# Optimization experiments

Measured on AMD Instinct MI355X. Metric: run time of the kernel, lower is better.

## Reference

```python
import jax, jax.numpy as jnp
import numpy as np

L, D, H, B, SX, SY, VS, VT = 6, 1024, 16, 4, 512, 512, 32000, 32000
DK = D // H
FF = 4 * D
EPS = 1e-3          # LayerNorm eps (added to std, not var)
SCALE_EMB = float(np.sqrt(D))
NEG = -1e30         # stands in for -inf; fully-masked rows are zeroed after softmax


def pos_encoding(length, d):
    # tensor2tensor-style sinusoid: [sin | cos] concatenated along channels
    nt = d // 2
    lti = np.log(1e4) / (nt - 1)
    inv = np.exp(np.arange(nt) * -lti)
    st = np.arange(length)[:, None] * inv[None, :]
    return jnp.asarray(np.concatenate([np.sin(st), np.cos(st)], axis=1), jnp.float32)


def layer_norm(z, a, b):
    # faithful to the torch module: uses unbiased std (ddof=1) and divides by (std + eps)
    mu = z.mean(-1, keepdims=True)
    sig = jnp.sqrt(((z - mu) ** 2).sum(-1, keepdims=True) / (z.shape[-1] - 1))
    return (z - mu) / (sig + EPS) * a + b


def mha(xq, xkv, wq, wk, wv, wo, mask):
    # xq: (b, lq, D), xkv: (b, lk, D); head-chunking of channel dim == reshape to (H, DK)
    b, lq, _ = xq.shape
    q = (xq @ wq.T).reshape(b, lq, H, DK)
    k = (xkv @ wk.T).reshape(b, -1, H, DK)
    v = (xkv @ wv.T).reshape(b, -1, H, DK)
    s = jnp.einsum('bqhd,bkhd->bhqk', q, k) * (1.0 / np.sqrt(DK))
    m = mask[:, None, :, :]
    s = jnp.where(m, s, NEG)
    att = jax.nn.softmax(s, axis=-1)
    att = att * m.any(-1, keepdims=True)  # replicates NaN->0 for fully masked rows
    c = jnp.einsum('bhqk,bkhd->bqhd', att, v).reshape(b, lq, D)
    return c @ wo.T


def setup_inputs():
    key = jax.random.key(0)
    ks = jax.random.split(key, 10)
    s = 0.02
    emb_x = (jax.random.normal(ks[0], (VS, D), jnp.float32) * s).at[0].set(0.0)  # padding_idx=0
    emb_y = (jax.random.normal(ks[1], (VT, D), jnp.float32) * s).at[0].set(0.0)
    return {
        'emb_x': emb_x, 'emb_y': emb_y,
        'enc_qkvo': jax.random.normal(ks[2], (L, 4, D, D), jnp.float32) * s,
        'enc_ln_s': jnp.ones((L, 2, D), jnp.float32), 'enc_ln_b': jnp.zeros((L, 2, D), jnp.float32),
        'enc_w1': jax.random.normal(ks[3], (L, FF, D), jnp.float32) * s, 'enc_b1': jnp.zeros((L, FF), jnp.float32),
        'enc_w2': jax.random.normal(ks[4], (L, D, FF), jnp.float32) * s, 'enc_b2': jnp.zeros((L, D), jnp.float32),
        'dec_qkvo': jax.random.normal(ks[5], (L, 8, D, D), jnp.float32) * s,
        'dec_ln_s': jnp.ones((L, 3, D), jnp.float32), 'dec_ln_b': jnp.zeros((L, 3, D), jnp.float32),
        'dec_w1': jax.random.normal(ks[6], (L, FF, D), jnp.float32) * s, 'dec_b1': jnp.zeros((L, FF), jnp.float32),
        'dec_w2': jax.random.normal(ks[7], (L, D, FF), jnp.float32) * s, 'dec_b2': jnp.zeros((L, D), jnp.float32),
        'x_block': jax.random.randint(ks[8], (B, SX), 0, VS),
        'y_block': jax.random.randint(ks[9], (B, SY), 0, VT),
    }


def reference(emb_x, emb_y, enc_qkvo, enc_ln_s, enc_ln_b, enc_w1, enc_b1, enc_w2, enc_b2,
              dec_qkvo, dec_ln_s, dec_ln_b, dec_w1, dec_b1, dec_w2, dec_b2, x_block, y_block):
    # internal layout (b, len, D); torch code uses (b, D, len) -- math is identical
    ex = emb_x[x_block] * SCALE_EMB + pos_encoding(SX, D)[None]
    ey = emb_y[y_block] * SCALE_EMB + pos_encoding(SY, D)[None]
    xv = x_block != 0
    yv = y_block != 0
    xx = xv[:, :, None] & xv[:, None, :]                                   # (B, qx, kx)
    xy = yv[:, :, None] & xv[:, None, :]                                   # (B, qy, kx)
    yy = (yv[:, :, None] & yv[:, None, :]) & jnp.tril(jnp.ones((SY, SY), bool))[None]
    e = ex
    for i in range(L):
        sub = mha(e, e, enc_qkvo[i, 0], enc_qkvo[i, 1], enc_qkvo[i, 2], enc_qkvo[i, 3], xx)
        e = layer_norm(e + sub, enc_ln_s[i, 0], enc_ln_b[i, 0])
        sub = jax.nn.relu(e @ enc_w1[i].T + enc_b1[i]) @ enc_w2[i].T + enc_b2[i]
        e = layer_norm(e + sub, enc_ln_s[i, 1], enc_ln_b[i, 1])
    z = e
    e = ey
    for i in range(L):
        sub = mha(e, e, dec_qkvo[i, 0], dec_qkvo[i, 1], dec_qkvo[i, 2], dec_qkvo[i, 3], yy)
        e = layer_norm(e + sub, dec_ln_s[i, 0], dec_ln_b[i, 0])
        sub = mha(e, z, dec_qkvo[i, 4], dec_qkvo[i, 5], dec_qkvo[i, 6], dec_qkvo[i, 7], xy)
        e = layer_norm(e + sub, dec_ln_s[i, 1], dec_ln_b[i, 1])
        sub = jax.nn.relu(e @ dec_w1[i].T + dec_b1[i]) @ dec_w2[i].T + dec_b2[i]
        e = layer_norm(e + sub, dec_ln_s[i, 2], dec_ln_b[i, 2])
    return e @ emb_y.T  # tied output projection -> (B, SY, VT)
```

## Files before the change

kernel.cpp:

```cpp
#include <hip/hip_runtime.h>

typedef unsigned short u16;
typedef float f32x4 __attribute__((ext_vector_type(4)));
typedef __bf16 bf16x8 __attribute__((ext_vector_type(8)));
typedef u16 u16x8 __attribute__((ext_vector_type(8)));

#define DEV __device__ __forceinline__

DEV u16 f2bf(float f) {
  unsigned u = __builtin_bit_cast(unsigned, f);
  u += 0x7fffu + ((u >> 16) & 1u);
  return (u16)(u >> 16);
}

DEV float wsum(float v) {
#pragma unroll
  for (int o = 32; o > 0; o >>= 1) v += __shfl_xor(v, o, 64);
  return v;
}
DEV float gmax16(float v) {
#pragma unroll
  for (int o = 8; o > 0; o >>= 1) v = fmaxf(v, __shfl_xor(v, o, 64));
  return v;
}
DEV float gsum16(float v) {
#pragma unroll
  for (int o = 8; o > 0; o >>= 1) v += __shfl_xor(v, o, 64);
  return v;
}

DEV void gld16(const void* g, void* l) {
  __builtin_amdgcn_global_load_lds((const __attribute__((address_space(1))) void*)g,
                                   (__attribute__((address_space(3))) void*)l, 16, 0, 0);
}

template <int N>
DEV void vwait() {
  if constexpr (N == 0) asm volatile("s_waitcnt vmcnt(0)" ::: "memory");
  else if constexpr (N == 2) asm volatile("s_waitcnt vmcnt(2)" ::: "memory");
  else if constexpr (N == 4) asm volatile("s_waitcnt vmcnt(4)" ::: "memory");
  else asm volatile("s_waitcnt vmcnt(6)" ::: "memory");
}

DEV void remap_bxy(int& bx, int& by) {
  const int gx = gridDim.x, gy = gridDim.y;
  const int flat = blockIdx.y * gx + blockIdx.x;
  const int nwg = gx * gy;
  const int q = nwg >> 3, r = nwg & 7;
  const int xcd = flat & 7, li = flat >> 3;
  const int wg = (xcd < r ? xcd * (q + 1) : r * (q + 1) + (xcd - r) * q) + li;
  by = wg % gy;
  bx = wg / gy;
}

template <int BM, int BN, int MODE, int W, int BK>
__global__ __launch_bounds__(256, W) void gemm_k(
    const u16* __restrict__ A, const u16* __restrict__ B, int lda, int ldb, int K,
    float alpha, const float* __restrict__ bias, const float* __restrict__ resid,
    float* __restrict__ Cf, int ldc, u16* __restrict__ Cb, u16* __restrict__ qp,
    u16* __restrict__ kp, u16* __restrict__ vp, int n_off) {
  constexpr int FM = BM / 32, FN = BN / 32;
  constexpr int CHA = BM / 8, CHT = (BM + BN) / 8;
  constexpr int KCH = BK / 64;
  __shared__ u16 lds[2][(BM + BN) * BK];
  const int lane = threadIdx.x & 63, wid = threadIdx.x >> 6;
  const int wr = wid >> 1, wc = wid & 1;
  int bx, by;
  remap_bxy(bx, by);
  const u16* gA = A + (long)(by * BM) * lda;
  const u16* gB = B + (long)(bx * BN) * ldb;

  const f32x4 zero4 = {0.f, 0.f, 0.f, 0.f};
  f32x4 acc[FM][FN];
#pragma unroll
  for (int m = 0; m < FM; ++m)
#pragma unroll
    for (int n = 0; n < FN; ++n) acc[m][n] = zero4;

  const int r8 = lane >> 3, sl = lane & 7;

  auto stage = [&](int buf, int kt) {
#pragma unroll
    for (int sub = 0; sub < KCH; ++sub) {
      const int kb = kt * BK + (sub << 6);
      u16* lbase = &lds[buf][sub * (BM + BN) * 64];
#pragma unroll
      for (int c0 = 0; c0 < CHT; c0 += 4) {
        const int c = c0 + wid;
        u16* l = lbase + (c << 9);
        const u16* g;
        if (c < CHA) {
          int r = (c << 3) + r8;
          g = gA + (long)r * lda + kb + ((sl ^ (r & 7)) << 3);
        } else {
          int r = ((c - CHA) << 3) + r8;
          g = gB + (long)r * ldb + kb + ((sl ^ (r & 7)) << 3);
        }
        gld16(g, l);
      }
    }
  };

  const int KT = K / BK;
  stage(0, 0);
  __syncthreads();
  int cur = 0;
  for (int kt = 0; kt < KT; ++kt) {
    if (kt + 1 < KT) stage(cur ^ 1, kt + 1);
#pragma unroll
    for (int q = 0; q < 2 * KCH; ++q) {
      const int kh = q >> 1, kl = q & 1;
      const u16* lA = &lds[cur][kh * (BM + BN) * 64];
      const u16* lB = lA + (BM << 6);
      bf16x8 af[FM], bv[FN];
#pragma unroll
      for (int m = 0; m < FM; ++m) {
        int r = wr * (BM / 2) + m * 16 + (lane & 15);
        int slot = ((kl << 2) | (lane >> 4)) ^ (r & 7);
        af[m] = *(const bf16x8*)(lA + (r << 6) + (slot << 3));
      }
#pragma unroll
      for (int n = 0; n < FN; ++n) {
        int r = wc * (BN / 2) + n * 16 + (lane & 15);
        int slot = ((kl << 2) | (lane >> 4)) ^ (r & 7);
        bv[n] = *(const bf16x8*)(lB + (r << 6) + (slot << 3));
      }
#pragma unroll
      for (int m = 0; m < FM; ++m)
#pragma unroll
        for (int n = 0; n < FN; ++n)
          acc[m][n] = __builtin_amdgcn_mfma_f32_16x16x32_bf16(af[m], bv[n], acc[m][n], 0, 0, 0);
    }
    __syncthreads();
    cur ^= 1;
  }

  const int rb = by * BM + wr * (BM / 2) + ((lane >> 4) << 2);
  const int cb = bx * BN + wc * (BN / 2) + (lane & 15);
  if constexpr (MODE == 2) {
    const bool isV = (bx * BN + n_off) >= 2048;
    if (isV) {
      __syncthreads();
      u16* T = (u16*)&lds[0][0];
      constexpr int TS = BM + 8;
#pragma unroll
      for (int m = 0; m < FM; ++m)
#pragma unroll
        for (int n = 0; n < FN; ++n) {
          int cl = wc * (BN / 2) + n * 16 + (lane & 15);
#pragma unroll
          for (int j = 0; j < 4; ++j) {
            int rl = wr * (BM / 2) + m * 16 + ((lane >> 4) << 2) + j;
            T[cl * TS + rl] = f2bf(acc[m][n][j]);
          }
        }
      __syncthreads();
      const int vcb = bx * BN + n_off - 2048;
      const int b = (by * BM) >> 9, s0 = (by * BM) & 511;
#pragma unroll
      for (int p = 0; p < BM * BN / 2048; ++p) {
        int idx = p * 2048 + threadIdx.x * 8;
        int dl = idx / BM, slx = idx & (BM - 1);
        u16x8 o;
#pragma unroll
        for (int e = 0; e < 8; ++e) o[e] = T[dl * TS + slx + e];
        int vc = vcb + dl;
        *(u16x8*)(vp + (((long)b * 16 + (vc >> 6)) * 64 + (vc & 63)) * 512 + s0 + slx) = o;
      }
    } else {
#pragma unroll
      for (int m = 0; m < FM; ++m)
#pragma unroll
        for (int n = 0; n < FN; ++n)
#pragma unroll
          for (int j = 0; j < 4; ++j) {
            const int row = rb + m * 16 + j;
            const int np = cb + n * 16 + n_off;
            const int sel = np >> 10, dim = np & 1023;
            long base = (((long)(row >> 9) * 16 + (dim >> 6)) * 512 + (row & 511)) * 64 + (dim & 63);
            u16 val = f2bf(acc[m][n][j]);
            if (sel == 0) qp[base] = val;
            else kp[base] = val;
          }
    }
  } else {
#pragma unroll
    for (int m = 0; m < FM; ++m)
#pragma unroll
      for (int n = 0; n < FN; ++n)
#pragma unroll
        for (int j = 0; j < 4; ++j) {
          const int row = rb + m * 16 + j;
          const int col = cb + n * 16;
          float v = acc[m][n][j];
          if constexpr (MODE == 0) {
            float r = v * alpha;
            if (bias) r += bias[col];
            if (resid) r += resid[(long)row * ldc + col];
            Cf[(long)row * ldc + col] = r;
          } else {
            Cb[(long)row * ldc + col] = f2bf(fmaxf(v + bias[col], 0.f));
          }
        }
  }
}

__global__ __launch_bounds__(512, 1) void gemm256_k(
    const u16* __restrict__ A, const u16* __restrict__ B, int lda, int ldb, int K,
    float* __restrict__ Cf, int ldc) {
  __shared__ u16 As[2][256 * 64];
  __shared__ u16 Bs[2][256 * 64];
  const int lane = threadIdx.x & 63, wid = threadIdx.x >> 6;
  const int wr = wid >> 2, wc = wid & 3;
  int bx, by;
  remap_bxy(bx, by);
  const u16* gA = A + (long)(by * 256) * lda;
  const u16* gB = B + (long)(bx * 256) * ldb;

  const f32x4 z4 = {0.f, 0.f, 0.f, 0.f};
  f32x4 acc[8][4];
#pragma unroll
  for (int m = 0; m < 8; ++m)
#pragma unroll
    for (int n = 0; n < 4; ++n) acc[m][n] = z4;

  const int ssl = lane & 7;

  auto stageH = [&](int t, int h) {
    const int kb = t << 6;
    const int buf = t & 1;
    const bool isA = (h == 0) || (h == 3);
    u16* ldsb = isA ? &As[buf][0] : &Bs[buf][0];
    const u16* gsrc = isA ? gA : gB;
    const int ld = isA ? lda : ldb;
    const int rbase = (h >= 2) ? 128 : 0;
#pragma unroll
    for (int rr = 0; rr < 2; ++rr) {
      const int r0 = rbase + rr * 64 + (wid << 3);
      const int r = r0 + (lane >> 3);
      gld16(gsrc + (long)r * ld + kb + ((ssl ^ (r & 7)) << 3), ldsb + (r0 << 6));
    }
  };

  const int KT = K >> 6;
  stageH(0, 0);
  stageH(0, 1);
  stageH(0, 2);
  stageH(0, 3);

  for (int t = 0; t < KT; ++t) {
    const int buf = t & 1;
    const bool more = (t + 1 < KT);
    const u16* lA = &As[buf][0];
    const u16* lB = &Bs[buf][0];
    bf16x8 af[4][2], bvl[2][2], bvh[2][2];

    vwait<4>();
    __builtin_amdgcn_s_barrier();
    __builtin_amdgcn_sched_barrier(0);
#pragma unroll
    for (int m = 0; m < 4; ++m)
#pragma unroll
      for (int kk = 0; kk < 2; ++kk) {
        int r = wr * 64 + m * 16 + (lane & 15);
        int sg = ((kk << 2) | (lane >> 4)) ^ (r & 7);
        af[m][kk] = *(const bf16x8*)(lA + (r << 6) + (sg << 3));
      }
#pragma unroll
    for (int n = 0; n < 2; ++n)
#pragma unroll
      for (int kk = 0; kk < 2; ++kk) {
        int c = wc * 32 + n * 16 + (lane & 15);
        int sg = ((kk << 2) | (lane >> 4)) ^ (c & 7);
        bvl[n][kk] = *(const bf16x8*)(lB + (c << 6) + (sg << 3));
      }
    if (more) stageH(t + 1, 0);
    __builtin_amdgcn_s_setprio(1);
#pragma unroll
    for (int kk = 0; kk < 2; ++kk)
#pragma unroll
      for (int m = 0; m < 4; ++m)
#pragma unroll
        for (int n = 0; n < 2; ++n)
          acc[m][n] = __builtin_amdgcn_mfma_f32_16x16x32_bf16(af[m][kk], bvl[n][kk], acc[m][n], 0, 0, 0);
    __builtin_amdgcn_s_setprio(0);

    if (more) vwait<4>();
    else vwait<2>();
    __builtin_amdgcn_s_barrier();
    __builtin_amdgcn_sched_barrier(0);
#pragma unroll
    for (int n = 0; n < 2; ++n)
#pragma unroll
      for (int kk = 0; kk < 2; ++kk) {
        int c = 128 + wc * 32 + n * 16 + (lane & 15);
        int sg = ((kk << 2) | (lane >> 4)) ^ (c & 7);
        bvh[n][kk] = *(const bf16x8*)(lB + (c << 6) + (sg << 3));
      }
    if (more) stageH(t + 1, 1);
    __builtin_amdgcn_s_setprio(1);
#pragma unroll
    for (int kk = 0; kk < 2; ++kk)
#pragma unroll
      for (int m = 0; m < 4; ++m)
#pragma unroll
        for (int n = 0; n < 2; ++n)
          acc[m][2 + n] = __builtin_amdgcn_mfma_f32_16x16x32_bf16(af[m][kk], bvh[n][kk], acc[m][2 + n], 0, 0, 0);
    __builtin_amdgcn_s_setprio(0);

    if (more) vwait<4>();
    else vwait<0>();
    __builtin_amdgcn_s_barrier();
    __builtin_amdgcn_sched_barrier(0);
#pragma unroll
    for (int m = 0; m < 4; ++m)
#pragma unroll
      for (int kk = 0; kk < 2; ++kk) {
        int r = 128 + wr * 64 + m * 16 + (lane & 15);
        int sg = ((kk << 2) | (lane >> 4)) ^ (r & 7);
        af[m][kk] = *(const bf16x8*)(lA + (r << 6) + (sg << 3));
      }
    if (more) stageH(t + 1, 2);
    __builtin_amdgcn_s_setprio(1);
#pragma unroll
    for (int kk = 0; kk < 2; ++kk)
#pragma unroll
      for (int m = 0; m < 4; ++m)
#pragma unroll
        for (int n = 0; n < 2; ++n)
          acc[4 + m][2 + n] = __builtin_amdgcn_mfma_f32_16x16x32_bf16(af[m][kk], bvh[n][kk], acc[4 + m][2 + n], 0, 0, 0);
    __builtin_amdgcn_s_setprio(0);

    __builtin_amdgcn_s_barrier();
    __builtin_amdgcn_sched_barrier(0);
    if (more) stageH(t + 1, 3);
    __builtin_amdgcn_s_setprio(1);
#pragma unroll
    for (int kk = 0; kk < 2; ++kk)
#pragma unroll
      for (int m = 0; m < 4; ++m)
#pragma unroll
        for (int n = 0; n < 2; ++n)
          acc[4 + m][n] = __builtin_amdgcn_mfma_f32_16x16x32_bf16(af[m][kk], bvl[n][kk], acc[4 + m][n], 0, 0, 0);
    __builtin_amdgcn_s_setprio(0);
  }

  const int rb = by * 256 + wr * 64 + ((lane >> 4) << 2);
  const int cb = bx * 256 + wc * 32 + (lane & 15);
#pragma unroll
  for (int mi = 0; mi < 8; ++mi)
#pragma unroll
    for (int ni = 0; ni < 4; ++ni)
#pragma unroll
      for (int j = 0; j < 4; ++j) {
        int row = rb + (mi & 3) * 16 + ((mi >> 2) << 7) + j;
        int col = cb + (ni & 1) * 16 + ((ni >> 1) << 7);
        Cf[(long)row * ldc + col] = acc[mi][ni][j];
      }
}

template <int CAUSAL>
__global__ __launch_bounds__(512, 2) void fattn_k(
    const u16* __restrict__ Qg, const u16* __restrict__ Kg, const u16* __restrict__ Vtg,
    const int* __restrict__ qids, const int* __restrict__ kids, u16* __restrict__ ctx) {
  __shared__ u16 Qs[128 * 64];
  __shared__ u16 Ks[2][64 * 64];
  __shared__ u16 Vs[2][64 * 64];
  __shared__ u16 Ps[8][16 * 64];
  const int lane = threadIdx.x & 63, wid = threadIdx.x >> 6;
  const int qt = blockIdx.x, bh = blockIdx.y, b = bh >> 4, h = bh & 15;
  const int q0 = qt << 7;
  const u16* Qbase = Qg + ((long)bh * 512 + q0) * 64;
  const u16* Kbase = Kg + (long)bh * 512 * 64;
  const u16* Vbase = Vtg + (long)bh * 64 * 512;
  const int r8 = lane >> 3, sl = lane & 7;

#pragma unroll
  for (int c0 = 0; c0 < 16; c0 += 8) {
    int c = c0 + wid;
    int r = (c << 3) + r8;
    gld16(Qbase + (long)r * 64 + ((sl ^ (r & 7)) << 3), &Qs[c << 9]);
  }

  auto stageKV = [&](int buf, int kt) {
#pragma unroll
    for (int c0 = 0; c0 < 16; c0 += 8) {
      int c = c0 + wid;
      if (c < 8) {
        int r = (c << 3) + r8;
        gld16(Kbase + (long)(kt * 64 + r) * 64 + ((sl ^ (r & 7)) << 3), &Ks[buf][c << 9]);
      } else {
        int r = ((c - 8) << 3) + r8;
        gld16(Vbase + (long)r * 512 + kt * 64 + ((sl ^ (r & 7)) << 3), &Vs[buf][(c - 8) << 9]);
      }
    }
  };

  const int NKT = CAUSAL ? ((q0 >> 6) + 2) : 8;
  stageKV(0, 0);
  __syncthreads();

  const f32x4 z4 = {0.f, 0.f, 0.f, 0.f};
  f32x4 oacc[4];
  float mrun[4], lrun[4];
  bool qv[4];
#pragma unroll
  for (int j = 0; j < 4; ++j) {
    mrun[j] = -3e38f;
    lrun[j] = 0.f;
    int qg = q0 + wid * 16 + ((lane >> 4) << 2) + j;
    qv[j] = qids[(b << 9) + qg] != 0;
  }
#pragma unroll
  for (int nd = 0; nd < 4; ++nd) oacc[nd] = z4;

  int cur = 0;
  for (int kt = 0; kt < NKT; ++kt) {
    if (kt + 1 < NKT) stageKV(cur ^ 1, kt + 1);
    f32x4 s[4];
#pragma unroll
    for (int n = 0; n < 4; ++n) s[n] = z4;
    __builtin_amdgcn_s_setprio(1);
#pragma unroll
    for (int kk = 0; kk < 2; ++kk) {
      bf16x8 aq, bk[4];
      int r = wid * 16 + (lane & 15);
      int slot = ((kk << 2) | (lane >> 4)) ^ (r & 7);
      aq = *(const bf16x8*)&Qs[(r << 6) + (slot << 3)];
#pragma unroll
      for (int n = 0; n < 4; ++n) {
        int c = n * 16 + (lane & 15);
        int slt = ((kk << 2) | (lane >> 4)) ^ (c & 7);
        bk[n] = *(const bf16x8*)&Ks[cur][(c << 6) + (slt << 3)];
      }
#pragma unroll
      for (int n = 0; n < 4; ++n)
        s[n] = __builtin_amdgcn_mfma_f32_16x16x32_bf16(aq, bk[n], s[n], 0, 0, 0);
    }
    __builtin_amdgcn_s_setprio(0);
    bool kvld[4];
#pragma unroll
    for (int n = 0; n < 4; ++n)
      kvld[n] = kids[(b << 9) + (kt << 6) + (n << 4) + (lane & 15)] != 0;
    float mx[4];
#pragma unroll
    for (int j = 0; j < 4; ++j) {
      mx[j] = -3e38f;
      int qg = q0 + wid * 16 + ((lane >> 4) << 2) + j;
#pragma unroll
      for (int n = 0; n < 4; ++n) {
        int colg = (kt << 6) + (n << 4) + (lane & 15);
        bool ok = qv[j] && kvld[n] && (!CAUSAL || colg <= qg);
        float sv = ok ? s[n][j] * 0.125f : -3e38f;
        s[n][j] = sv;
        mx[j] = fmaxf(mx[j], sv);
      }
      mx[j] = gmax16(mx[j]);
    }
#pragma unroll
    for (int j = 0; j < 4; ++j) {
      float mn = fmaxf(mrun[j], mx[j]);
      float f = __expf(mrun[j] - mn);
      mrun[j] = mn;
      float ps = 0.f;
#pragma unroll
      for (int n = 0; n < 4; ++n) {
        float sv = s[n][j];
        float p = (sv > -1e37f) ? __expf(sv - mn) : 0.f;
        s[n][j] = p;
        ps += p;
      }
      ps = gsum16(ps);
      lrun[j] = lrun[j] * f + ps;
#pragma unroll
      for (int nd = 0; nd < 4; ++nd) oacc[nd][j] *= f;
    }
#pragma unroll
    for (int n = 0; n < 4; ++n)
#pragma unroll
      for (int j = 0; j < 4; ++j) {
        int rl = ((lane >> 4) << 2) + j;
        int slot = ((n << 1) | ((lane >> 3) & 1)) ^ (rl & 7);
        Ps[wid][(rl << 6) + (slot << 3) + (lane & 7)] = f2bf(s[n][j]);
      }
    __builtin_amdgcn_s_setprio(1);
#pragma unroll
    for (int kk = 0; kk < 2; ++kk) {
      bf16x8 pa, vv[4];
      int r = lane & 15;
      int slot = ((kk << 2) | (lane >> 4)) ^ (r & 7);
      pa = *(const bf16x8*)&Ps[wid][(r << 6) + (slot << 3)];
#pragma unroll
      for (int nd = 0; nd < 4; ++nd) {
        int rv = (nd << 4) + (lane & 15);
        int slt = ((kk << 2) | (lane >> 4)) ^ (rv & 7);
        vv[nd] = *(const bf16x8*)&Vs[cur][(rv << 6) + (slt << 3)];
      }
#pragma unroll
      for (int nd = 0; nd < 4; ++nd)
        oacc[nd] = __builtin_amdgcn_mfma_f32_16x16x32_bf16(pa, vv[nd], oacc[nd], 0, 0, 0);
    }
    __builtin_amdgcn_s_setprio(0);
    __syncthreads();
    cur ^= 1;
  }
#pragma unroll
  for (int j = 0; j < 4; ++j) {
    float inv = (lrun[j] > 0.f) ? 1.0f / lrun[j] : 0.f;
    int qg = q0 + wid * 16 + ((lane >> 4) << 2) + j;
    long rowb = (((long)(b << 9) + qg) * 16 + h) * 64;
#pragma unroll
    for (int nd = 0; nd < 4; ++nd) {
      int d = (nd << 4) + (lane & 15);
      ctx[rowb + d] = f2bf(oacc[nd][j] * inv);
    }
  }
}

__global__ __launch_bounds__(256) void embed_k(const int* __restrict__ ids,
                                               const float* __restrict__ emb,
                                               float* __restrict__ xo, u16* __restrict__ bfo) {
  const int tok = blockIdx.x, t = threadIdx.x;
  const int s = tok & 511;
  const long id = ids[tok];
  const int d = t * 4;
  float4 ev = *(const float4*)(emb + id * 1024 + d);
  float o[4] = {ev.x * 32.f, ev.y * 32.f, ev.z * 32.f, ev.w * 32.f};
#pragma unroll
  for (int j = 0; j < 4; ++j) {
    int dd = d + j, di = dd & 511;
    float ang = (float)s * expf(-(float)di * 0.0180241494559220821f);
    o[j] += (dd < 512) ? sinf(ang) : cosf(ang);
  }
  *(float4*)(xo + (long)tok * 1024 + d) = make_float4(o[0], o[1], o[2], o[3]);
  ushort4 ob = {f2bf(o[0]), f2bf(o[1]), f2bf(o[2]), f2bf(o[3])};
  *(ushort4*)(bfo + (long)tok * 1024 + d) = ob;
}

__global__ __launch_bounds__(256) void ln_k(const float* __restrict__ vin,
                                            const float* __restrict__ gam,
                                            const float* __restrict__ bet,
                                            float* __restrict__ xo, u16* __restrict__ bfo) {
  __shared__ float red[8];
  const int row = blockIdx.x, t = threadIdx.x;
  const float4 xv = *(const float4*)(vin + (long)row * 1024 + t * 4);
  float v0 = xv.x, v1 = xv.y, v2 = xv.z, v3 = xv.w;
  float sm = wsum(v0 + v1 + v2 + v3);
  if ((t & 63) == 0) red[t >> 6] = sm;
  __syncthreads();
  const float mu = (red[0] + red[1] + red[2] + red[3]) * (1.0f / 1024.0f);
  const float d0 = v0 - mu, d1 = v1 - mu, d2 = v2 - mu, d3 = v3 - mu;
  float ss = wsum(d0 * d0 + d1 * d1 + d2 * d2 + d3 * d3);
  if ((t & 63) == 0) red[4 + (t >> 6)] = ss;
  __syncthreads();
  const float sig = sqrtf((red[4] + red[5] + red[6] + red[7]) * (1.0f / 1023.0f));
  const float inv = 1.0f / (sig + 0.001f);
  const float4 g4 = *(const float4*)(gam + t * 4);
  const float4 b4 = *(const float4*)(bet + t * 4);
  const float o0 = d0 * inv * g4.x + b4.x, o1 = d1 * inv * g4.y + b4.y;
  const float o2 = d2 * inv * g4.z + b4.z, o3 = d3 * inv * g4.w + b4.w;
  *(float4*)(xo + (long)row * 1024 + t * 4) = make_float4(o0, o1, o2, o3);
  ushort4 ob = {f2bf(o0), f2bf(o1), f2bf(o2), f2bf(o3)};
  *(ushort4*)(bfo + (long)row * 1024 + t * 4) = ob;
}

__global__ void cvt_k(const float* __restrict__ src, u16* __restrict__ dst, int n4) {
  for (int i = blockIdx.x * 256 + threadIdx.x; i < n4; i += gridDim.x * 256) {
    float4 v = ((const float4*)src)[i];
    ushort4 o = {f2bf(v.x), f2bf(v.y), f2bf(v.z), f2bf(v.w)};
    ((ushort4*)dst)[i] = o;
  }
}

__global__ void cvt3_k(const float* __restrict__ s0, int n0, const float* __restrict__ s1,
                       int n1, const float* __restrict__ s2, int n2, u16* __restrict__ dst) {
  const int tot = n0 + n1 + n2;
  for (int i = blockIdx.x * 256 + threadIdx.x; i < tot; i += gridDim.x * 256) {
    const float* s;
    int j;
    if (i < n0) { s = s0; j = i; }
    else if (i < n0 + n1) { s = s1; j = i - n0; }
    else { s = s2; j = i - n0 - n1; }
    float4 v = ((const float4*)s)[j];
    ushort4 o = {f2bf(v.x), f2bf(v.y), f2bf(v.z), f2bf(v.w)};
    ((ushort4*)dst)[i] = o;
  }
}

extern "C" void kernel_launch(void* const* d_in, const int* in_sizes, int n_in, void* d_out,
                              int out_size, void* d_ws, size_t ws_size, hipStream_t stream) {
  (void)in_sizes; (void)n_in; (void)out_size;
  const float* emb_x = (const float*)d_in[0];
  const float* emb_y = (const float*)d_in[1];
  const float* enc_qkvo = (const float*)d_in[2];
  const float* enc_ln_s = (const float*)d_in[3];
  const float* enc_ln_b = (const float*)d_in[4];
  const float* enc_w1 = (const float*)d_in[5];
  const float* enc_b1 = (const float*)d_in[6];
  const float* enc_w2 = (const float*)d_in[7];
  const float* enc_b2 = (const float*)d_in[8];
  const float* dec_qkvo = (const float*)d_in[9];
  const float* dec_ln_s = (const float*)d_in[10];
  const float* dec_ln_b = (const float*)d_in[11];
  const float* dec_w1 = (const float*)d_in[12];
  const float* dec_b1 = (const float*)d_in[13];
  const float* dec_w2 = (const float*)d_in[14];
  const float* dec_b2 = (const float*)d_in[15];
  const int* x_block = (const int*)d_in[16];
  const int* y_block = (const int*)d_in[17];

  const long TOK = 2048, Dm = 1024, M1 = 1048576;
  char* p = (char*)d_ws;
  auto alloc = [&](long bytes) { char* r = p; p += (bytes + 255) & ~255L; return r; };
  float* e32 = (float*)alloc(TOK * Dm * 4);
  float* sub = (float*)alloc(TOK * Dm * 4);
  u16* ebf = (u16*)alloc(TOK * Dm * 2);
  u16* zbf = (u16*)alloc(TOK * Dm * 2);
  u16* qb = (u16*)alloc(TOK * Dm * 2);
  u16* kb = (u16*)alloc(TOK * Dm * 2);
  u16* vtb = (u16*)alloc(TOK * Dm * 2);
  u16* ctx = (u16*)alloc(TOK * Dm * 2);
  u16* hbuf = (u16*)alloc(TOK * 4096 * 2);
  u16* wbuf = (u16*)alloc(16L * M1 * 2);
  u16* embyb = (u16*)alloc(32000L * 1024 * 2);
  if ((size_t)(p - (char*)d_ws) > ws_size) return;

  auto gemmF = [&](const u16* A, const u16* Bw, int M, int N, int K, int lda, int ldb,
                   float alpha, const float* bias, const float* resid, float* C, int ldc) {
    dim3 g(N / 64, M / 64);
    gemm_k<64, 64, 0, 2, 128><<<g, 256, 0, stream>>>(A, Bw, lda, ldb, K, alpha, bias, resid,
                                                     C, ldc, nullptr, nullptr, nullptr,
                                                     nullptr, 0);
  };
  auto gemmRelu = [&](const u16* A, const u16* Bw, const float* bias, u16* C) {
    dim3 g(32, 16);
    gemm_k<128, 128, 1, 2, 64><<<g, 256, 0, stream>>>(A, Bw, 1024, 1024, 1024, 1.f, bias,
                                                      nullptr, nullptr, 4096, C, nullptr,
                                                      nullptr, nullptr, 0);
  };
  auto gemmQKV = [&](const u16* A, const u16* Bw, int N, int n_off) {
    if (N >= 2048) {
      dim3 g(N / 128, 32);
      gemm_k<64, 128, 2, 3, 64><<<g, 256, 0, stream>>>(A, Bw, 1024, 1024, 1024, 1.f, nullptr,
                                                       nullptr, nullptr, 0, nullptr, qb, kb,
                                                       vtb, n_off);
    } else {
      dim3 g(N / 64, 32);
      gemm_k<64, 64, 2, 4, 64><<<g, 256, 0, stream>>>(A, Bw, 1024, 1024, 1024, 1.f, nullptr,
                                                      nullptr, nullptr, 0, nullptr, qb, kb,
                                                      vtb, n_off);
    }
  };
  auto attn = [&](const int* qids, const int* kids, int causal) {
    if (causal)
      fattn_k<1><<<dim3(4, 64), 512, 0, stream>>>(qb, kb, vtb, qids, kids, ctx);
    else
      fattn_k<0><<<dim3(4, 64), 512, 0, stream>>>(qb, kb, vtb, qids, kids, ctx);
  };
  auto lnorm = [&](const float* g, const float* b) {
    ln_k<<<2048, 256, 0, stream>>>(sub, g, b, e32, ebf);
  };

  cvt_k<<<2048, 256, 0, stream>>>(emb_y, embyb, 32000 * 1024 / 4);

  embed_k<<<2048, 256, 0, stream>>>(x_block, emb_x, e32, ebf);
  for (int i = 0; i < 6; ++i) {
    cvt3_k<<<2048, 256, 0, stream>>>(enc_qkvo + (long)i * 4 * M1, (int)M1,
                                     enc_w1 + (long)i * 4 * M1, (int)M1,
                                     enc_w2 + (long)i * 4 * M1, (int)M1, wbuf);
    gemmQKV(ebf, wbuf, 3072, 0);
    attn(x_block, x_block, 0);
    gemmF(ctx, wbuf + 3L * M1, 2048, 1024, 1024, 1024, 1024, 1.f, nullptr, e32, sub, 1024);
    lnorm(enc_ln_s + (i * 2 + 0) * 1024, enc_ln_b + (i * 2 + 0) * 1024);
    gemmRelu(ebf, wbuf + 4L * M1, enc_b1 + i * 4096, hbuf);
    gemmF(hbuf, wbuf + 8L * M1, 2048, 1024, 4096, 4096, 4096, 1.f, enc_b2 + i * 1024, e32,
          sub, 1024);
    lnorm(enc_ln_s + (i * 2 + 1) * 1024, enc_ln_b + (i * 2 + 1) * 1024);
  }
  hipMemcpyAsync(zbf, ebf, TOK * Dm * 2, hipMemcpyDeviceToDevice, stream);

  embed_k<<<2048, 256, 0, stream>>>(y_block, emb_y, e32, ebf);
  for (int i = 0; i < 6; ++i) {
    cvt3_k<<<2048, 256, 0, stream>>>(dec_qkvo + (long)i * 8 * M1, (int)(2 * M1),
                                     dec_w1 + (long)i * 4 * M1, (int)M1,
                                     dec_w2 + (long)i * 4 * M1, (int)M1, wbuf);
    gemmQKV(ebf, wbuf, 3072, 0);
    attn(y_block, y_block, 1);
    gemmF(ctx, wbuf + 3L * M1, 2048, 1024, 1024, 1024, 1024, 1.f, nullptr, e32, sub, 1024);
    lnorm(dec_ln_s + (i * 3 + 0) * 1024, dec_ln_b + (i * 3 + 0) * 1024);
    gemmQKV(ebf, wbuf + 4L * M1, 1024, 0);
    gemmQKV(zbf, wbuf + 5L * M1, 2048, 1024);
    attn(y_block, x_block, 0);
    gemmF(ctx, wbuf + 7L * M1, 2048, 1024, 1024, 1024, 1024, 1.f, nullptr, e32, sub, 1024);
    lnorm(dec_ln_s + (i * 3 + 1) * 1024, dec_ln_b + (i * 3 + 1) * 1024);
    gemmRelu(ebf, wbuf + 8L * M1, dec_b1 + i * 4096, hbuf);
    gemmF(hbuf, wbuf + 12L * M1, 2048, 1024, 4096, 4096, 4096, 1.f, dec_b2 + i * 1024, e32,
          sub, 1024);
    lnorm(dec_ln_s + (i * 3 + 2) * 1024, dec_ln_b + (i * 3 + 2) * 1024);
  }
  gemm256_k<<<dim3(125, 8), 512, 0, stream>>>(ebf, embyb, 1024, 1024, 1024,
                                              (float*)d_out, 32000);
}
```

Measured before the change: 2.276 ms.

## Add quarter-staged pipelined 128x128 GEMM for FFN and triple-buffer attention KV

Adds a new 128x128 GEMM kernel that splits each K-tile stage into four half-tile loads interleaved with quarter MFMA blocks, using vmcnt waits and raw barriers instead of full syncthreads. The FFN up-projection with ReLU now uses it. The attention kernel moves from double- to triple-buffered K/V with prefetch two tiles ahead and fine-grained vmcnt waits. The intent is to hide global-load latency behind MFMA work. The cost is more LDS use in attention, which may reduce occupancy, and more complex synchronization.

```diff
diff --git a/kernel.cpp b/kernel.cpp
--- a/kernel.cpp
+++ b/kernel.cpp
@@ -205,6 +205,167 @@
   }
 }
 
+template <int MODE>
+__global__ __launch_bounds__(256, 2) void gemm128p_k(
+    const u16* __restrict__ A, const u16* __restrict__ B, int lda, int ldb, int K,
+    const float* __restrict__ bias, float* __restrict__ Cf, int ldc,
+    u16* __restrict__ Cb) {
+  __shared__ u16 As[2][128 * 64];
+  __shared__ u16 Bs[2][128 * 64];
+  const int lane = threadIdx.x & 63, wid = threadIdx.x >> 6;
+  const int wr = wid >> 1, wc = wid & 1;
+  int bx, by;
+  remap_bxy(bx, by);
+  const u16* gA = A + (long)(by * 128) * lda;
+  const u16* gB = B + (long)(bx * 128) * ldb;
+
+  const f32x4 z4 = {0.f, 0.f, 0.f, 0.f};
+  f32x4 acc[4][4];
+#pragma unroll
+  for (int m = 0; m < 4; ++m)
+#pragma unroll
+    for (int n = 0; n < 4; ++n) acc[m][n] = z4;
+
+  const int ssl = lane & 7;
+
+  auto stageH = [&](int t, int h) {
+    const int kb = t << 6;
+    const int buf = t & 1;
+    const bool isA = (h == 0) || (h == 3);
+    u16* ldsb = isA ? &As[buf][0] : &Bs[buf][0];
+    const u16* gsrc = isA ? gA : gB;
+    const int ld = isA ? lda : ldb;
+    const int rbase = (h >= 2) ? 64 : 0;
+#pragma unroll
+    for (int rr = 0; rr < 2; ++rr) {
+      const int r0 = rbase + rr * 32 + (wid << 3);
+      const int r = r0 + (lane >> 3);
+      gld16(gsrc + (long)r * ld + kb + ((ssl ^ (r & 7)) << 3), ldsb + (r0 << 6));
+    }
+  };
+
+  const int KT = K >> 6;
+  stageH(0, 0);
+  stageH(0, 1);
+  stageH(0, 2);
+  stageH(0, 3);
+
+  for (int t = 0; t < KT; ++t) {
+    const int buf = t & 1;
+    const bool more = (t + 1 < KT);
+    const u16* lA = &As[buf][0];
+    const u16* lB = &Bs[buf][0];
+    bf16x8 af[2][2], bvl[2][2], bvh[2][2];
+
+    vwait<4>();
+    __builtin_amdgcn_s_barrier();
+    __builtin_amdgcn_sched_barrier(0);
+#pragma unroll
+    for (int m = 0; m < 2; ++m)
+#pragma unroll
+      for (int kk = 0; kk < 2; ++kk) {
+        int r = wr * 32 + m * 16 + (lane & 15);
+        int sg = ((kk << 2) | (lane >> 4)) ^ (r & 7);
+        af[m][kk] = *(const bf16x8*)(lA + (r << 6) + (sg << 3));
+      }
+#pragma unroll
+    for (int n = 0; n < 2; ++n)
+#pragma unroll
+      for (int kk = 0; kk < 2; ++kk) {
+        int c = wc * 32 + n * 16 + (lane & 15);
+        int sg = ((kk << 2) | (lane >> 4)) ^ (c & 7);
+        bvl[n][kk] = *(const bf16x8*)(lB + (c << 6) + (sg << 3));
+      }
+    if (more) stageH(t + 1, 0);
+    __builtin_amdgcn_s_setprio(1);
+#pragma unroll
+    for (int kk = 0; kk < 2; ++kk)
+#pragma unroll
+      for (int m = 0; m < 2; ++m)
+#pragma unroll
+        for (int n = 0; n < 2; ++n)
+          acc[m][n] = __builtin_amdgcn_mfma_f32_16x16x32_bf16(af[m][kk], bvl[n][kk], acc[m][n], 0, 0, 0);
+    __builtin_amdgcn_s_setprio(0);
+
+    if (more) vwait<4>();
+    else vwait<2>();
+    __builtin_amdgcn_s_barrier();
+    __builtin_amdgcn_sched_barrier(0);
+#pragma unroll
+    for (int n = 0; n < 2; ++n)
+#pragma unroll
+      for (int kk = 0; kk < 2; ++kk) {
+        int c = 64 + wc * 32 + n * 16 + (lane & 15);
+        int sg = ((kk << 2) | (lane >> 4)) ^ (c & 7);
+        bvh[n][kk] = *(const bf16x8*)(lB + (c << 6) + (sg << 3));
+      }
+    if (more) stageH(t + 1, 1);
+    __builtin_amdgcn_s_setprio(1);
+#pragma unroll
+    for (int kk = 0; kk < 2; ++kk)
+#pragma unroll
+      for (int m = 0; m < 2; ++m)
+#pragma unroll
+        for (int n = 0; n < 2; ++n)
+          acc[m][2 + n] = __builtin_amdgcn_mfma_f32_16x16x32_bf16(af[m][kk], bvh[n][kk], acc[m][2 + n], 0, 0, 0);
+    __builtin_amdgcn_s_setprio(0);
+
+    if (more) vwait<4>();
+    else vwait<0>();
+    __builtin_amdgcn_s_barrier();
+    __builtin_amdgcn_sched_barrier(0);
+#pragma unroll
+    for (int m = 0; m < 2; ++m)
+#pragma unroll
+      for (int kk = 0; kk < 2; ++kk) {
+        int r = 64 + wr * 32 + m * 16 + (lane & 15);
+        int sg = ((kk << 2) | (lane >> 4)) ^ (r & 7);
+        af[m][kk] = *(const bf16x8*)(lA + (r << 6) + (sg << 3));
+      }
+    if (more) stageH(t + 1, 2);
+    __builtin_amdgcn_s_setprio(1);
+#pragma unroll
+    for (int kk = 0; kk < 2; ++kk)
+#pragma unroll
+      for (int m = 0; m < 2; ++m)
+#pragma unroll
+        for (int n = 0; n < 2; ++n)
+          acc[2 + m][2 + n] = __builtin_amdgcn_mfma_f32_16x16x32_bf16(af[m][kk], bvh[n][kk], acc[2 + m][2 + n], 0, 0, 0);
+    __builtin_amdgcn_s_setprio(0);
+
+    __builtin_amdgcn_s_barrier();
+    __builtin_amdgcn_sched_barrier(0);
+    if (more) stageH(t + 1, 3);
+    __builtin_amdgcn_s_setprio(1);
+#pragma unroll
+    for (int kk = 0; kk < 2; ++kk)
+#pragma unroll
+      for (int m = 0; m < 2; ++m)
+#pragma unroll
+        for (int n = 0; n < 2; ++n)
+          acc[2 + m][n] = __builtin_amdgcn_mfma_f32_16x16x32_bf16(af[m][kk], bvl[n][kk], acc[2 + m][n], 0, 0, 0);
+    __builtin_amdgcn_s_setprio(0);
+  }
+
+#pragma unroll
+  for (int mi = 0; mi < 4; ++mi)
+#pragma unroll
+    for (int ni = 0; ni < 4; ++ni)
+#pragma unroll
+      for (int j = 0; j < 4; ++j) {
+        int row = by * 128 + (mi >> 1) * 64 + wr * 32 + (mi & 1) * 16 + ((lane >> 4) << 2) + j;
+        int col = bx * 128 + (ni >> 1) * 64 + wc * 32 + (ni & 1) * 16 + (lane & 15);
+        float v = acc[mi][ni][j];
+        if constexpr (MODE == 1) {
+          Cb[(long)row * ldc + col] = f2bf(fmaxf(v + bias[col], 0.f));
+        } else {
+          float r = v;
+          if (bias) r += bias[col];
+          Cf[(long)row * ldc + col] = r;
+        }
+      }
+}
+
 __global__ __launch_bounds__(512, 1) void gemm256_k(
     const u16* __restrict__ A, const u16* __restrict__ B, int lda, int ldb, int K,
     float* __restrict__ Cf, int ldc) {
@@ -364,8 +525,8 @@
     const u16* __restrict__ Qg, const u16* __restrict__ Kg, const u16* __restrict__ Vtg,
     const int* __restrict__ qids, const int* __restrict__ kids, u16* __restrict__ ctx) {
   __shared__ u16 Qs[128 * 64];
-  __shared__ u16 Ks[2][64 * 64];
-  __shared__ u16 Vs[2][64 * 64];
+  __shared__ u16 Ks[3][64 * 64];
+  __shared__ u16 Vs[3][64 * 64];
   __shared__ u16 Ps[8][16 * 64];
   const int lane = threadIdx.x & 63, wid = threadIdx.x >> 6;
   const int qt = blockIdx.x, bh = blockIdx.y, b = bh >> 4, h = bh & 15;
@@ -398,7 +559,10 @@
 
   const int NKT = CAUSAL ? ((q0 >> 6) + 2) : 8;
   stageKV(0, 0);
-  __syncthreads();
+  if (NKT > 1) stageKV(1, 1);
+  if (NKT > 1) vwait<2>();
+  else vwait<0>();
+  __builtin_amdgcn_s_barrier();
 
   const f32x4 z4 = {0.f, 0.f, 0.f, 0.f};
   f32x4 oacc[4];
@@ -414,9 +578,9 @@
 #pragma unroll
   for (int nd = 0; nd < 4; ++nd) oacc[nd] = z4;
 
-  int cur = 0;
   for (int kt = 0; kt < NKT; ++kt) {
-    if (kt + 1 < NKT) stageKV(cur ^ 1, kt + 1);
+    const int cur = kt % 3;
+    if (kt + 2 < NKT) stageKV((kt + 2) % 3, kt + 2);
     f32x4 s[4];
 #pragma unroll
     for (int n = 0; n < 4; ++n) s[n] = z4;
@@ -501,8 +665,14 @@
         oacc[nd] = __builtin_amdgcn_mfma_f32_16x16x32_bf16(pa, vv[nd], oacc[nd], 0, 0, 0);
     }
     __builtin_amdgcn_s_setprio(0);
-    __syncthreads();
-    cur ^= 1;
+    const int ahead = NKT - 1 - kt;
+    if (ahead >= 2) {
+      vwait<2>();
+      __builtin_amdgcn_s_barrier();
+    } else if (ahead == 1) {
+      vwait<0>();
+      __builtin_amdgcn_s_barrier();
+    }
   }
 #pragma unroll
   for (int j = 0; j < 4; ++j) {
@@ -634,9 +804,7 @@
   };
   auto gemmRelu = [&](const u16* A, const u16* Bw, const float* bias, u16* C) {
     dim3 g(32, 16);
-    gemm_k<128, 128, 1, 2, 64><<<g, 256, 0, stream>>>(A, Bw, 1024, 1024, 1024, 1.f, bias,
-                                                      nullptr, nullptr, 4096, C, nullptr,
-                                                      nullptr, nullptr, 0);
+    gemm128p_k<1><<<g, 256, 0, stream>>>(A, Bw, 1024, 1024, 1024, bias, nullptr, 4096, C);
   };
   auto gemmQKV = [&](const u16* A, const u16* Bw, int N, int n_off) {
     if (N >= 2048) {
```

Measured after the change: 2.329 ms. 1.02x slower.
